# Optimization experiments

Hardware: AMD Instinct MI355X
Metric: run time of the kernel (lower is better)

The kernel has to match this reference:

```python
import jax, jax.numpy as jnp
import numpy as np

N_MIX = 5
PRUNE_LEFT, PRUNE_RIGHT = -50, 50


def setup_inputs() -> dict:
    key = jax.random.key(0)
    k = jax.random.split(key, 5)
    B, L, D, Q, H = 32, 8192, 256, 512, 256
    ctx = jax.random.normal(k[0], (B, L, D), dtype=jnp.float32)
    query = jax.random.normal(k[1], (B, Q), dtype=jnp.float32)
    W1 = jax.random.normal(k[2], (H, Q), dtype=jnp.float32) * (1.0 / np.sqrt(Q))
    b1 = jnp.zeros((H,), dtype=jnp.float32)
    W2 = jax.random.normal(k[3], (3 * N_MIX, H), dtype=jnp.float32) * (1.0 / np.sqrt(H))
    # bias init: alpha_bias=0, beta_bias=0, kappa_bias=-1
    b2 = jnp.concatenate([jnp.zeros(2 * N_MIX), jnp.full((N_MIX,), -1.0)]).astype(jnp.float32)
    return {"ctx": ctx, "query": query, "W1": W1, "b1": b1, "W2": W2, "b2": b2}


def reference(ctx, query, W1, b1, W2, b2):
    # ctx: (B, L, D), query: (B, Q)
    B, L, D = ctx.shape
    proj = jnp.tanh(query @ W1.T + b1)              # (B, H)
    stats = proj @ W2.T + b2                        # (B, 3*M)
    _alpha, _beta, _kappa = jnp.split(stats, 3, axis=1)  # each (B, M)
    alpha = jnp.exp(_alpha)
    beta = jnp.exp(_beta)
    kappa = jnp.exp(_kappa)                         # monotonic: + kappa_prev (zeros on first step)

    pos = jnp.arange(L, dtype=ctx.dtype)            # (L,)
    # prune_type='ind': per-(batch, mixture) window around round(kappa)
    center = jnp.round(jax.lax.stop_gradient(kappa))  # (B, M), detached like .data in torch
    left = center + PRUNE_LEFT
    right = center + PRUNE_RIGHT + 1
    prune_mask = ((pos[None, None, :] >= left[:, :, None]) &
                  (pos[None, None, :] < right[:, :, None])).astype(ctx.dtype)  # (B, M, L)

    diff = pos[None, None, :] - kappa[:, :, None]   # (B, M, L)
    score = alpha[:, :, None] * jnp.exp(-beta[:, :, None] * diff * diff)
    score = score * prune_mask
    p_ctx = jnp.sum(score, axis=1)                  # (B, L)

    expected_ctx = jnp.einsum('bl,bld->bd', p_ctx, ctx)  # (B, D)
    return expected_ctx, p_ctx
```

## Files before the change

kernel.cpp:

```cpp
#include <hip/hip_runtime.h>
#include <math.h>

#define BB 32
#define LL 8192
#define DD 256
#define QQ 512
#define HH 256
#define MM 5
#define PRUNE_LEFT  (-50)
#define PRUNE_RIGHT (50)

__device__ inline float wave_reduce_add(float v) {
    #pragma unroll
    for (int m = 1; m < 64; m <<= 1)
        v += __shfl_xor(v, m, 64);
    return v;
}

__global__ void __launch_bounds__(1024, 1) k_fused(
    const float* __restrict__ ctx,
    const float* __restrict__ query,
    const float* __restrict__ W1,
    const float* __restrict__ b1,
    const float* __restrict__ W2,
    const float* __restrict__ b2,
    float* __restrict__ expected,
    float* __restrict__ p_ctx)
{
    __shared__ float s_proj[HH];
    __shared__ float s_stats[3 * MM];
    __shared__ float s_p[LL];
    __shared__ float s_part[4][DD];

    const int b    = blockIdx.x;
    const int t    = threadIdx.x;
    const int lane = t & 63;
    const int w    = t >> 6;

    const float4* q4 = (const float4*)(query + (size_t)b * QQ);
    const float4 qa = q4[lane];
    const float4 qb = q4[64 + lane];
    const float4* W1_4 = (const float4*)W1;

    #pragma unroll
    for (int r = 0; r < 16; ++r) {
        const int h = w * 16 + r;
        const float4 wa = W1_4[(size_t)h * 128 + lane];
        const float4 wb = W1_4[(size_t)h * 128 + 64 + lane];
        float acc = wa.x * qa.x + wa.y * qa.y + wa.z * qa.z + wa.w * qa.w
                  + wb.x * qb.x + wb.y * qb.y + wb.z * qb.z + wb.w * qb.w;
        acc = wave_reduce_add(acc);
        if (lane == 0) s_proj[h] = tanhf(acc + b1[h]);
    }
    __syncthreads();

    if (w < 3 * MM) {
        const float4 pv = ((const float4*)s_proj)[lane];
        const float4 w2 = ((const float4*)W2)[(size_t)w * 64 + lane];
        float acc = w2.x * pv.x + w2.y * pv.y + w2.z * pv.z + w2.w * pv.w;
        acc = wave_reduce_add(acc);
        if (lane == 0) s_stats[w] = expf(acc + b2[w]);
    }
    __syncthreads();

    float alpha[MM], beta[MM], kappa[MM], cen[MM];
    #pragma unroll
    for (int m = 0; m < MM; ++m) {
        alpha[m] = s_stats[m];
        beta[m]  = s_stats[MM + m];
        kappa[m] = s_stats[2 * MM + m];
        cen[m]   = rintf(kappa[m]);
    }

    float* pb = p_ctx + (size_t)b * LL;
    #pragma unroll
    for (int l = t; l < LL; l += 1024) {
        const float pos = (float)l;
        float p = 0.f;
        #pragma unroll
        for (int m = 0; m < MM; ++m) {
            if (pos >= cen[m] + (float)PRUNE_LEFT && pos < cen[m] + (float)(PRUNE_RIGHT + 1)) {
                const float diff = pos - kappa[m];
                p += alpha[m] * expf(-beta[m] * diff * diff);
            }
        }
        s_p[l] = p;
        pb[l] = p;
    }

    float cmin = 1e30f, cmax = -1e30f;
    #pragma unroll
    for (int m = 0; m < MM; ++m) {
        cmin = fminf(cmin, cen[m]);
        cmax = fmaxf(cmax, cen[m]);
    }
    const float lof = fminf(fmaxf(0.f, cmin + (float)PRUNE_LEFT), (float)LL);
    const float hif = fminf(fmaxf(0.f, cmax + (float)(PRUNE_RIGHT + 1)), (float)LL);
    const int lo = (int)lof;
    const int hi = ((int)hif < lo) ? lo : (int)hif;

    __syncthreads();

    const int d  = t & 255;
    const int wq = t >> 8;
    const float* cb = ctx + (size_t)b * LL * DD;

    float acc = 0.f;
    #pragma unroll 4
    for (int r = lo + wq; r < hi; r += 4) {
        acc += s_p[r] * cb[(size_t)r * DD + d];
    }
    s_part[wq][d] = acc;
    __syncthreads();
    if (t < DD) {
        expected[(size_t)b * DD + t] =
            s_part[0][t] + s_part[1][t] + s_part[2][t] + s_part[3][t];
    }
}

extern "C" void kernel_launch(void* const* d_in, const int* in_sizes, int n_in,
                              void* d_out, int out_size, void* d_ws, size_t ws_size,
                              hipStream_t stream) {
    const float* ctx   = (const float*)d_in[0];
    const float* query = (const float*)d_in[1];
    const float* W1    = (const float*)d_in[2];
    const float* b1    = (const float*)d_in[3];
    const float* W2    = (const float*)d_in[4];
    const float* b2    = (const float*)d_in[5];

    float* out      = (float*)d_out;
    float* expected = out;
    float* p_ctx    = out + BB * DD;

    k_fused<<<BB, 1024, 0, stream>>>(ctx, query, W1, b1, W2, b2, expected, p_ctx);
}
```

Before: 17.87 us.

## Split projection into separate wide kernel and prefetch ctx rows early

The first MLP layer moves into its own kernel launched over 8x32 blocks, so the W1 matvec is spread across many CUs instead of 32 blocks of 1024 threads. The main kernel reads proj from workspace and issues an early prefetch of the first 128 rows of each batch's ctx slab into registers. A dummy asm use keeps those loads alive. This adds a second launch, a workspace round trip, and prefetches that only help when the pruning window lies in the first rows.

Measured after the change: 16.03 us. 10.3% less time.

```diff
diff --git a/kernel.cpp b/kernel.cpp
--- a/kernel.cpp
+++ b/kernel.cpp
@@ -17,22 +17,12 @@
     return v;
 }
 
-__global__ void __launch_bounds__(1024, 1) k_fused(
-    const float* __restrict__ ctx,
-    const float* __restrict__ query,
-    const float* __restrict__ W1,
-    const float* __restrict__ b1,
-    const float* __restrict__ W2,
-    const float* __restrict__ b2,
-    float* __restrict__ expected,
-    float* __restrict__ p_ctx)
-{
-    __shared__ float s_proj[HH];
-    __shared__ float s_stats[3 * MM];
-    __shared__ float s_p[LL];
-    __shared__ float s_part[4][DD];
-
-    const int b    = blockIdx.x;
+__global__ void __launch_bounds__(256) k_proj(const float* __restrict__ query,
+                                              const float* __restrict__ W1,
+                                              const float* __restrict__ b1,
+                                              float* __restrict__ proj_ws) {
+    const int b    = blockIdx.y;
+    const int c    = blockIdx.x;
     const int t    = threadIdx.x;
     const int lane = t & 63;
     const int w    = t >> 6;
@@ -43,19 +33,41 @@
     const float4* W1_4 = (const float4*)W1;
 
     #pragma unroll
-    for (int r = 0; r < 16; ++r) {
-        const int h = w * 16 + r;
+    for (int r = 0; r < 8; ++r) {
+        const int h = c * 32 + w * 8 + r;
         const float4 wa = W1_4[(size_t)h * 128 + lane];
         const float4 wb = W1_4[(size_t)h * 128 + 64 + lane];
         float acc = wa.x * qa.x + wa.y * qa.y + wa.z * qa.z + wa.w * qa.w
                   + wb.x * qb.x + wb.y * qb.y + wb.z * qb.z + wb.w * qb.w;
         acc = wave_reduce_add(acc);
-        if (lane == 0) s_proj[h] = tanhf(acc + b1[h]);
+        if (lane == 0) proj_ws[b * HH + h] = tanhf(acc + b1[h]);
     }
-    __syncthreads();
+}
+
+__global__ void __launch_bounds__(1024, 1) k_fused(
+    const float* __restrict__ ctx,
+    const float* __restrict__ W2,
+    const float* __restrict__ b2,
+    const float* __restrict__ proj_ws,
+    float* __restrict__ expected,
+    float* __restrict__ p_ctx)
+{
+    __shared__ float s_stats[3 * MM];
+    __shared__ float s_p[LL];
+    __shared__ float s_part[4][DD];
+
+    const int b    = blockIdx.x;
+    const int t    = threadIdx.x;
+    const int lane = t & 63;
+    const int w    = t >> 6;
+
+    const float4* cp = (const float4*)(ctx + (size_t)b * LL * DD);
+    float4 pf[8];
+    #pragma unroll
+    for (int i = 0; i < 8; ++i) pf[i] = cp[(size_t)i * 1024 + t];
 
     if (w < 3 * MM) {
-        const float4 pv = ((const float4*)s_proj)[lane];
+        const float4 pv = ((const float4*)(proj_ws + (size_t)b * HH))[lane];
         const float4 w2 = ((const float4*)W2)[(size_t)w * 64 + lane];
         float acc = w2.x * pv.x + w2.y * pv.y + w2.z * pv.z + w2.w * pv.w;
         acc = wave_reduce_add(acc);
@@ -99,6 +111,13 @@
     const int lo = (int)lof;
     const int hi = ((int)hif < lo) ? lo : (int)hif;
 
+    {
+        float keep = 0.f;
+        #pragma unroll
+        for (int i = 0; i < 8; ++i) keep += pf[i].x + pf[i].y + pf[i].z + pf[i].w;
+        asm volatile("" :: "v"(keep));
+    }
+
     __syncthreads();
 
     const int d  = t & 255;
@@ -131,6 +150,10 @@
     float* out      = (float*)d_out;
     float* expected = out;
     float* p_ctx    = out + BB * DD;
+    float* proj_ws  = (float*)d_ws;
 
-    k_fused<<<BB, 1024, 0, stream>>>(ctx, query, W1, b1, W2, b2, expected, p_ctx);
+    dim3 g1(8, BB);
+    k_proj<<<g1, 256, 0, stream>>>(query, W1, b1, proj_ws);
+
+    k_fused<<<BB, 1024, 0, stream>>>(ctx, W2, b2, proj_ws, expected, p_ctx);
 }
```
